# Performance work log

Measured on AMD Instinct MI355X. Metric: run time of the kernel, lower is better.

## Reference

```python
import jax, jax.numpy as jnp
import numpy as np

TAU = 0.5
EPS = 1e-8


def setup_inputs() -> dict:
    key = jax.random.key(0)
    k1, k2 = jax.random.split(key)
    N, D = 200000, 512
    z_pos = jax.random.normal(k1, (N, D), dtype=jnp.float32)
    W = jax.random.normal(k2, (D, D), dtype=jnp.float32) * (1.0 / np.sqrt(D))
    b = jnp.zeros((D,), dtype=jnp.float32)
    return {"z_pos": z_pos, "W": W, "b": b}


def reference(z_pos, W, b):
    # sample_centroid: softmax-weighted centroid (computed on detached embeddings)
    h = jax.lax.stop_gradient(z_pos)
    init_c = h.mean(axis=0)                              # [D]
    d2 = jnp.sum((h - init_c[None, :]) ** 2, axis=1)     # [N]
    w = jax.nn.softmax(-d2 / TAU)                        # [N]
    c = jnp.sum(h * w[:, None], axis=0)                  # [D]

    # SimNet: dist = 1 - cosine_similarity(proj(x), c)
    x_proj = z_pos @ W.T + b                             # [N, D]
    x_norm = jnp.maximum(jnp.linalg.norm(x_proj, axis=-1), EPS)  # [N]
    c_norm = jnp.maximum(jnp.linalg.norm(c), EPS)
    cos = (x_proj @ c) / (x_norm * c_norm)               # [N]
    dist = 1.0 - cos
    return dist
```

## Files before the change

### kernel.cpp

```cpp
#include <hip/hip_runtime.h>
#include <hip/hip_bf16.h>
#include <math.h>

#define DD 512
#define EPSF 1e-8f
#define BM 128
#define BN 128
#define BK 32
#define FBIG 3.402823466e+38f
#define NPART 2048

typedef __bf16 bf16_t;
typedef __bf16 bf16x4_t __attribute__((ext_vector_type(4)));
typedef __bf16 bf16x8_t __attribute__((ext_vector_type(8)));
typedef float f32x4 __attribute__((ext_vector_type(4)));

__device__ inline float bf2f(unsigned short u) {
    return __uint_as_float(((unsigned int)u) << 16);
}

__global__ void k_convW(const float* __restrict__ W, bf16_t* __restrict__ Wb) {
    int i = blockIdx.x * blockDim.x + threadIdx.x;
    float4 v = ((const float4*)W)[i];
    bf16x4_t o;
    o[0] = (bf16_t)v.x; o[1] = (bf16_t)v.y; o[2] = (bf16_t)v.z; o[3] = (bf16_t)v.w;
    ((bf16x4_t*)Wb)[i] = o;
}

template<bool CONV>
__global__ void k_colsum(const float* __restrict__ z, bf16_t* __restrict__ zb,
                         float* __restrict__ part, int N, int rpb) {
    int t = threadIdx.x;
    int b = blockIdx.x;
    int col4 = t & 127, sub = t >> 7;
    int r0 = b * rpb, r1 = min(r0 + rpb, N);
    const float4* z4 = (const float4*)z;
    float4 acc = make_float4(0.f, 0.f, 0.f, 0.f);
    #pragma unroll 4
    for (int r = r0 + sub; r < r1; r += 2) {
        float4 v = z4[(size_t)r * 128 + col4];
        if (CONV) {
            bf16x4_t o;
            o[0] = (bf16_t)v.x; o[1] = (bf16_t)v.y; o[2] = (bf16_t)v.z; o[3] = (bf16_t)v.w;
            ((bf16x4_t*)zb)[(size_t)r * 128 + col4] = o;
        }
        acc.x += v.x; acc.y += v.y; acc.z += v.z; acc.w += v.w;
    }
    __shared__ float4 sm[128];
    if (sub == 1) sm[col4] = acc;
    __syncthreads();
    if (sub == 0) {
        float4 o = sm[col4];
        acc.x += o.x; acc.y += o.y; acc.z += o.z; acc.w += o.w;
        ((float4*)(part + (size_t)b * DD))[col4] = acc;
    }
}

__global__ void k_wcolsum_f(const float* __restrict__ z, const float* __restrict__ d2,
                            const float* __restrict__ d2min, const float* __restrict__ sinvp,
                            float* __restrict__ part, int N, int rpb) {
    int t = threadIdx.x;
    int b = blockIdx.x;
    int col4 = t & 127, sub = t >> 7;
    int r0 = b * rpb, r1 = min(r0 + rpb, N);
    float m  = d2min[0];
    float is = sinvp[0];
    const float4* z4 = (const float4*)z;
    float4 acc = make_float4(0.f, 0.f, 0.f, 0.f);
    #pragma unroll 4
    for (int r = r0 + sub; r < r1; r += 2) {
        float w = __expf(-2.0f * (d2[r] - m)) * is;
        float4 v = z4[(size_t)r * 128 + col4];
        acc.x += w * v.x; acc.y += w * v.y; acc.z += w * v.z; acc.w += w * v.w;
    }
    __shared__ float4 sm[128];
    if (sub == 1) sm[col4] = acc;
    __syncthreads();
    if (sub == 0) {
        float4 o = sm[col4];
        acc.x += o.x; acc.y += o.y; acc.z += o.z; acc.w += o.w;
        ((float4*)(part + (size_t)b * DD))[col4] = acc;
    }
}

__global__ void k_wcolsum_b(const bf16_t* __restrict__ zb, const float* __restrict__ d2,
                            const float* __restrict__ d2min, const float* __restrict__ sinvp,
                            float* __restrict__ part, int N, int rpb) {
    int t = threadIdx.x;
    int b = blockIdx.x;
    int col4 = t & 127, sub = t >> 7;
    int r0 = b * rpb, r1 = min(r0 + rpb, N);
    float m  = d2min[0];
    float is = sinvp[0];
    const ushort4* z4 = (const ushort4*)zb;
    float4 acc = make_float4(0.f, 0.f, 0.f, 0.f);
    #pragma unroll 8
    for (int r = r0 + sub; r < r1; r += 2) {
        float w = __expf(-2.0f * (d2[r] - m)) * is;
        ushort4 u = z4[(size_t)r * 128 + col4];
        acc.x += w * bf2f(u.x); acc.y += w * bf2f(u.y);
        acc.z += w * bf2f(u.z); acc.w += w * bf2f(u.w);
    }
    __shared__ float4 sm[128];
    if (sub == 1) sm[col4] = acc;
    __syncthreads();
    if (sub == 0) {
        float4 o = sm[col4];
        acc.x += o.x; acc.y += o.y; acc.z += o.z; acc.w += o.w;
        ((float4*)(part + (size_t)b * DD))[col4] = acc;
    }
}

__global__ void k_reduceP(const float* __restrict__ part, float* __restrict__ outv, float scale) {
    __shared__ float sm[256];
    int j = blockIdx.x;
    int t = threadIdx.x;
    float s = 0.f;
    #pragma unroll
    for (int p = 0; p < NPART / 256; ++p) s += part[(size_t)(p * 256 + t) * DD + j];
    sm[t] = s;
    __syncthreads();
    for (int st = 128; st > 0; st >>= 1) {
        if (t < st) sm[t] += sm[t + st];
        __syncthreads();
    }
    if (t == 0) outv[j] = sm[0] * scale;
}

__global__ void k_d2s(const float* __restrict__ z, const float* __restrict__ cbar,
                      float* __restrict__ d2, float* __restrict__ mpart,
                      float* __restrict__ spart, int N) {
    int t = threadIdx.x;
    int lane = t & 63, wv = t >> 6;
    int l15 = lane & 15, r4 = lane >> 4;
    const float4* c4 = (const float4*)cbar;
    float4 cf[8];
    #pragma unroll
    for (int q = 0; q < 8; ++q) cf[q] = c4[q * 16 + l15];
    int gw = (blockIdx.x * 256 + t) >> 6;
    int nw = (gridDim.x * 256) >> 6;
    float m = FBIG, s = 0.f;
    #pragma unroll 2
    for (int r = gw * 4 + r4; r < N; r += nw * 4) {
        const float4* zr = (const float4*)(z + (size_t)r * DD);
        float sum = 0.f;
        #pragma unroll
        for (int q = 0; q < 8; ++q) {
            float4 v = zr[q * 16 + l15];
            float d;
            d = v.x - cf[q].x; sum += d * d;
            d = v.y - cf[q].y; sum += d * d;
            d = v.z - cf[q].z; sum += d * d;
            d = v.w - cf[q].w; sum += d * d;
        }
        #pragma unroll
        for (int off = 1; off < 16; off <<= 1) sum += __shfl_xor(sum, off, 64);
        if (l15 == 0) d2[r] = sum;
        float nm = fminf(m, sum);
        s = s * __expf(-2.0f * (m - nm)) + __expf(-2.0f * (sum - nm));
        m = nm;
    }
    #pragma unroll
    for (int off = 16; off < 64; off <<= 1) {
        float m2 = __shfl_xor(m, off, 64);
        float s2 = __shfl_xor(s, off, 64);
        float nm = fminf(m, m2);
        s = s * __expf(-2.0f * (m - nm)) + s2 * __expf(-2.0f * (m2 - nm));
        m = nm;
    }
    __shared__ float smm[4], sms[4];
    if (lane == 0) { smm[wv] = m; sms[wv] = s; }
    __syncthreads();
    if (t == 0) {
        float M = fminf(fminf(smm[0], smm[1]), fminf(smm[2], smm[3]));
        float S = 0.f;
        #pragma unroll
        for (int i = 0; i < 4; ++i) S += sms[i] * __expf(-2.0f * (smm[i] - M));
        mpart[blockIdx.x] = M;
        spart[blockIdx.x] = S;
    }
}

__global__ void k_combine(const float* __restrict__ mpart, const float* __restrict__ spart,
                          float* __restrict__ d2min, float* __restrict__ sinvp) {
    __shared__ float smm[256], sms[256];
    int t = threadIdx.x;
    float M = FBIG, S = 0.f;
    for (int i = t; i < NPART; i += 256) {
        float m2 = mpart[i], s2 = spart[i];
        float nm = fminf(M, m2);
        S = S * __expf(-2.0f * (M - nm)) + s2 * __expf(-2.0f * (m2 - nm));
        M = nm;
    }
    smm[t] = M; sms[t] = S;
    __syncthreads();
    for (int st = 128; st > 0; st >>= 1) {
        if (t < st) {
            float m2 = smm[t + st], s2 = sms[t + st];
            float nm = fminf(smm[t], m2);
            sms[t] = sms[t] * __expf(-2.0f * (smm[t] - nm)) + s2 * __expf(-2.0f * (m2 - nm));
            smm[t] = nm;
        }
        __syncthreads();
    }
    if (t == 0) { d2min[0] = smm[0]; sinvp[0] = 1.0f / sms[0]; }
}

__global__ void k_cnorm(const float* __restrict__ cvec, float* __restrict__ outp) {
    __shared__ float sm[512];
    float v = cvec[threadIdx.x];
    sm[threadIdx.x] = v * v;
    __syncthreads();
    for (int st = 256; st > 0; st >>= 1) {
        if (threadIdx.x < st) sm[threadIdx.x] += sm[threadIdx.x + st];
        __syncthreads();
    }
    if (threadIdx.x == 0) outp[0] = 1.0f / fmaxf(sqrtf(sm[0]), EPSF);
}

template<bool ZB>
__global__ __launch_bounds__(256, 4) void k_gemm(
    const float* __restrict__ z, const bf16_t* __restrict__ zb,
    const bf16_t* __restrict__ Wb, const float* __restrict__ bvec,
    const float* __restrict__ cvec, float* __restrict__ sqp, float* __restrict__ dtp,
    int N, int npad)
{
    __shared__ bf16_t As[BM * BK];
    __shared__ bf16_t Bs[BN * BK];
    __shared__ float psq[BM][2];
    __shared__ float pdt[BM][2];

    const int t    = threadIdx.x;
    const int lane = t & 63;
    const int wv   = t >> 6;
    const int wr   = wv >> 1;
    const int wc   = wv & 1;
    const int quad = lane >> 4;
    const int l15  = lane & 15;
    const int cb   = blockIdx.x;
    const int row0 = blockIdx.y * BM;

    const bf16_t* bp = Wb + (size_t)(cb * BN + (t >> 2)) * DD + (t & 3) * 8;
    const bf16_t* ap = zb + (size_t)(row0 + (t >> 2)) * DD + (t & 3) * 8;

    const int arow = t >> 1;
    const int ah   = t & 1;
    int rowe = row0 + arow; if (rowe >= N) rowe = N - 1;
    const float4* zp4 = (const float4*)(z + (size_t)rowe * DD + ah * 16);

    f32x4 acc[4][4];
    #pragma unroll
    for (int a = 0; a < 4; ++a)
        #pragma unroll
        for (int b = 0; b < 4; ++b) acc[a][b] = (f32x4){0.f, 0.f, 0.f, 0.f};

    float4 v0, v1, v2, v3;
    if (!ZB) { v0 = zp4[0]; v1 = zp4[1]; v2 = zp4[2]; v3 = zp4[3]; }

    for (int kc = 0; kc < DD; kc += BK) {
        if (kc) __syncthreads();

        #pragma unroll
        for (int q = 0; q < 2; ++q) {
            int ldsoff = __builtin_amdgcn_readfirstlane(q * 4096 + wv * 1024);
            __builtin_amdgcn_global_load_lds(
                (const __attribute__((address_space(1))) unsigned int*)(const void*)(bp + (size_t)q * 64 * DD + kc),
                (__attribute__((address_space(3))) unsigned int*)(void*)((char*)Bs + ldsoff),
                16, 0, 0);
        }
        if (ZB) {
            #pragma unroll
            for (int q = 0; q < 2; ++q) {
                int ldsoff = __builtin_amdgcn_readfirstlane(q * 4096 + wv * 1024);
                __builtin_amdgcn_global_load_lds(
                    (const __attribute__((address_space(1))) unsigned int*)(const void*)(ap + (size_t)q * 64 * DD + kc),
                    (__attribute__((address_space(3))) unsigned int*)(void*)((char*)As + ldsoff),
                    16, 0, 0);
            }
        } else {
            bf16x8_t lo, hi;
            lo[0]=(bf16_t)v0.x; lo[1]=(bf16_t)v0.y; lo[2]=(bf16_t)v0.z; lo[3]=(bf16_t)v0.w;
            lo[4]=(bf16_t)v1.x; lo[5]=(bf16_t)v1.y; lo[6]=(bf16_t)v1.z; lo[7]=(bf16_t)v1.w;
            hi[0]=(bf16_t)v2.x; hi[1]=(bf16_t)v2.y; hi[2]=(bf16_t)v2.z; hi[3]=(bf16_t)v2.w;
            hi[4]=(bf16_t)v3.x; hi[5]=(bf16_t)v3.y; hi[6]=(bf16_t)v3.z; hi[7]=(bf16_t)v3.w;
            *(bf16x8_t*)(As + arow * BK + ah * 16)     = lo;
            *(bf16x8_t*)(As + arow * BK + ah * 16 + 8) = hi;
        }

        __syncthreads();

        if (!ZB && kc + BK < DD) {
            int kf = (kc + BK) >> 2;
            v0 = zp4[kf]; v1 = zp4[kf + 1]; v2 = zp4[kf + 2]; v3 = zp4[kf + 3];
        }

        bf16x8_t af[4];
        #pragma unroll
        for (int rt = 0; rt < 4; ++rt)
            af[rt] = *(const bf16x8_t*)(As + (wr * 64 + rt * 16 + l15) * BK + quad * 8);
        #pragma unroll
        for (int ct = 0; ct < 4; ++ct) {
            bf16x8_t bfv = *(const bf16x8_t*)(Bs + (wc * 64 + ct * 16 + l15) * BK + quad * 8);
            #pragma unroll
            for (int rt = 0; rt < 4; ++rt)
                acc[rt][ct] = __builtin_amdgcn_mfma_f32_16x16x32_bf16(af[rt], bfv, acc[rt][ct], 0, 0, 0);
        }
    }

    float bc[4], cc[4];
    #pragma unroll
    for (int ct = 0; ct < 4; ++ct) {
        int col = cb * BN + wc * 64 + ct * 16 + l15;
        bc[ct] = bvec[col];
        cc[ct] = cvec[col];
    }
    #pragma unroll
    for (int rt = 0; rt < 4; ++rt) {
        #pragma unroll
        for (int rg = 0; rg < 4; ++rg) {
            float sq = 0.f, dt = 0.f;
            #pragma unroll
            for (int ct = 0; ct < 4; ++ct) {
                float x = acc[rt][ct][rg] + bc[ct];
                sq += x * x;
                dt += x * cc[ct];
            }
            #pragma unroll
            for (int off = 1; off < 16; off <<= 1) {
                sq += __shfl_xor(sq, off, 64);
                dt += __shfl_xor(dt, off, 64);
            }
            if (l15 == 0) {
                int rl = wr * 64 + rt * 16 + quad * 4 + rg;
                psq[rl][wc] = sq;
                pdt[rl][wc] = dt;
            }
        }
    }
    __syncthreads();
    if (t < BM) {
        int r = row0 + t;
        if (r < N) {
            sqp[(size_t)cb * npad + r] = psq[t][0] + psq[t][1];
            dtp[(size_t)cb * npad + r] = pdt[t][0] + pdt[t][1];
        }
    }
}

__global__ void k_final(const float* __restrict__ sqp, const float* __restrict__ dtp,
                        const float* __restrict__ cninv, float* __restrict__ out,
                        int N, int npad) {
    int r = blockIdx.x * blockDim.x + threadIdx.x;
    if (r < N) {
        float sq = sqp[r] + sqp[(size_t)npad + r] + sqp[2 * (size_t)npad + r] + sqp[3 * (size_t)npad + r];
        float dt = dtp[r] + dtp[(size_t)npad + r] + dtp[2 * (size_t)npad + r] + dtp[3 * (size_t)npad + r];
        out[r] = 1.0f - dt * cninv[0] / fmaxf(sqrtf(sq), EPSF);
    }
}

extern "C" void kernel_launch(void* const* d_in, const int* in_sizes, int n_in,
                              void* d_out, int out_size, void* d_ws, size_t ws_size,
                              hipStream_t stream)
{
    const float* z = (const float*)d_in[0];
    const float* W = (const float*)d_in[1];
    const float* b = (const float*)d_in[2];
    float* out = (float*)d_out;
    int N = in_sizes[0] / DD;
    int npad = ((N + BM - 1) / BM) * BM;

    float* ws = (float*)d_ws;
    size_t off = 0;
    float* part  = ws + off; off += (size_t)NPART * DD;
    float* cbar  = ws + off; off += DD;
    float* d2    = ws + off; off += (size_t)npad;
    float* mpart = ws + off; off += NPART;
    float* spart = ws + off; off += NPART;
    float* d2min = ws + off; off += 1;
    float* sinvp = ws + off; off += 1;
    float* cvec  = ws + off; off += DD;
    float* cninv = ws + off; off += 1;
    off = (off + 3) & ~(size_t)3;
    float* sqp   = ws + off; off += (size_t)4 * npad;
    float* dtp   = ws + off; off += (size_t)4 * npad;
    bf16_t* Wb   = (bf16_t*)(ws + off); off += (size_t)DD * DD / 2;
    bf16_t* zb   = (bf16_t*)(ws + off);
    size_t need_bytes = (off + (size_t)npad * DD / 2) * sizeof(float);
    const bool use_zb = ws_size >= need_bytes;

    int rpb = (N + NPART - 1) / NPART;

    k_convW<<<256, 256, 0, stream>>>(W, Wb);
    if (use_zb) k_colsum<true ><<<NPART, 256, 0, stream>>>(z, zb, part, N, rpb);
    else        k_colsum<false><<<NPART, 256, 0, stream>>>(z, zb, part, N, rpb);
    k_reduceP<<<DD, 256, 0, stream>>>(part, cbar, 1.0f / (float)N);
    k_d2s<<<NPART, 256, 0, stream>>>(z, cbar, d2, mpart, spart, N);
    k_combine<<<1, 256, 0, stream>>>(mpart, spart, d2min, sinvp);
    if (use_zb) k_wcolsum_b<<<NPART, 256, 0, stream>>>(zb, d2, d2min, sinvp, part, N, rpb);
    else        k_wcolsum_f<<<NPART, 256, 0, stream>>>(z,  d2, d2min, sinvp, part, N, rpb);
    k_reduceP<<<DD, 256, 0, stream>>>(part, cvec, 1.0f);
    k_cnorm<<<1, DD, 0, stream>>>(cvec, cninv);
    dim3 grid(4, npad / BM);
    if (use_zb) k_gemm<true ><<<grid, 256, 0, stream>>>(z, zb, Wb, b, cvec, sqp, dtp, N, npad);
    else        k_gemm<false><<<grid, 256, 0, stream>>>(z, zb, Wb, b, cvec, sqp, dtp, N, npad);
    k_final<<<(N + 255) / 256, 256, 0, stream>>>(sqp, dtp, cninv, out, N, npad);
}
```

Baseline: 904.0 us.

## Fuse distance, online softmax and weighted centroid into one pass over z

Merges the d2/softmax-stats kernel and the separate weighted column-sum kernel into a single pass. It keeps an online-softmax running max and rescales per-thread weighted accumulators, so z (or its bf16 copy) is read once instead of twice. The per-block partial centroids are then rescaled by per-block weights in a new weighted reduction kernel. The GEMM epilogue also shortens its shuffle reduction and stores more partials in shared memory. This costs more registers in the fused kernel (eight float4 accumulators plus loaded values) and rescaling work whenever the running max changes.

```diff
diff --git a/kernel.cpp b/kernel.cpp
--- a/kernel.cpp
+++ b/kernel.cpp
@@ -14,10 +14,6 @@
 typedef __bf16 bf16x4_t __attribute__((ext_vector_type(4)));
 typedef __bf16 bf16x8_t __attribute__((ext_vector_type(8)));
 typedef float f32x4 __attribute__((ext_vector_type(4)));
-
-__device__ inline float bf2f(unsigned short u) {
-    return __uint_as_float(((unsigned int)u) << 16);
-}
 
 __global__ void k_convW(const float* __restrict__ W, bf16_t* __restrict__ Wb) {
     int i = blockIdx.x * blockDim.x + threadIdx.x;
@@ -56,61 +52,6 @@
     }
 }
 
-__global__ void k_wcolsum_f(const float* __restrict__ z, const float* __restrict__ d2,
-                            const float* __restrict__ d2min, const float* __restrict__ sinvp,
-                            float* __restrict__ part, int N, int rpb) {
-    int t = threadIdx.x;
-    int b = blockIdx.x;
-    int col4 = t & 127, sub = t >> 7;
-    int r0 = b * rpb, r1 = min(r0 + rpb, N);
-    float m  = d2min[0];
-    float is = sinvp[0];
-    const float4* z4 = (const float4*)z;
-    float4 acc = make_float4(0.f, 0.f, 0.f, 0.f);
-    #pragma unroll 4
-    for (int r = r0 + sub; r < r1; r += 2) {
-        float w = __expf(-2.0f * (d2[r] - m)) * is;
-        float4 v = z4[(size_t)r * 128 + col4];
-        acc.x += w * v.x; acc.y += w * v.y; acc.z += w * v.z; acc.w += w * v.w;
-    }
-    __shared__ float4 sm[128];
-    if (sub == 1) sm[col4] = acc;
-    __syncthreads();
-    if (sub == 0) {
-        float4 o = sm[col4];
-        acc.x += o.x; acc.y += o.y; acc.z += o.z; acc.w += o.w;
-        ((float4*)(part + (size_t)b * DD))[col4] = acc;
-    }
-}
-
-__global__ void k_wcolsum_b(const bf16_t* __restrict__ zb, const float* __restrict__ d2,
-                            const float* __restrict__ d2min, const float* __restrict__ sinvp,
-                            float* __restrict__ part, int N, int rpb) {
-    int t = threadIdx.x;
-    int b = blockIdx.x;
-    int col4 = t & 127, sub = t >> 7;
-    int r0 = b * rpb, r1 = min(r0 + rpb, N);
-    float m  = d2min[0];
-    float is = sinvp[0];
-    const ushort4* z4 = (const ushort4*)zb;
-    float4 acc = make_float4(0.f, 0.f, 0.f, 0.f);
-    #pragma unroll 8
-    for (int r = r0 + sub; r < r1; r += 2) {
-        float w = __expf(-2.0f * (d2[r] - m)) * is;
-        ushort4 u = z4[(size_t)r * 128 + col4];
-        acc.x += w * bf2f(u.x); acc.y += w * bf2f(u.y);
-        acc.z += w * bf2f(u.z); acc.w += w * bf2f(u.w);
-    }
-    __shared__ float4 sm[128];
-    if (sub == 1) sm[col4] = acc;
-    __syncthreads();
-    if (sub == 0) {
-        float4 o = sm[col4];
-        acc.x += o.x; acc.y += o.y; acc.z += o.z; acc.w += o.w;
-        ((float4*)(part + (size_t)b * DD))[col4] = acc;
-    }
-}
-
 __global__ void k_reduceP(const float* __restrict__ part, float* __restrict__ outv, float scale) {
     __shared__ float sm[256];
     int j = blockIdx.x;
@@ -127,83 +68,152 @@
     if (t == 0) outv[j] = sm[0] * scale;
 }
 
-__global__ void k_d2s(const float* __restrict__ z, const float* __restrict__ cbar,
-                      float* __restrict__ d2, float* __restrict__ mpart,
-                      float* __restrict__ spart, int N) {
+__global__ __launch_bounds__(256, 4) void k_d2w(
+    const float* __restrict__ z, const float* __restrict__ cbar,
+    float* __restrict__ part, float* __restrict__ mpart,
+    float* __restrict__ spart, int N)
+{
+    __shared__ float4 cs[128];
+    __shared__ float4 vsm[4][128];
+    __shared__ float wm[4], wsv[4];
     int t = threadIdx.x;
     int lane = t & 63, wv = t >> 6;
     int l15 = lane & 15, r4 = lane >> 4;
-    const float4* c4 = (const float4*)cbar;
-    float4 cf[8];
-    #pragma unroll
-    for (int q = 0; q < 8; ++q) cf[q] = c4[q * 16 + l15];
+    if (t < 128) cs[t] = ((const float4*)cbar)[t];
+    __syncthreads();
+
     int gw = (blockIdx.x * 256 + t) >> 6;
     int nw = (gridDim.x * 256) >> 6;
     float m = FBIG, s = 0.f;
-    #pragma unroll 2
+    float4 acc[8];
+    #pragma unroll
+    for (int q = 0; q < 8; ++q) acc[q] = make_float4(0.f, 0.f, 0.f, 0.f);
+
     for (int r = gw * 4 + r4; r < N; r += nw * 4) {
         const float4* zr = (const float4*)(z + (size_t)r * DD);
+        float4 vv[8];
         float sum = 0.f;
         #pragma unroll
         for (int q = 0; q < 8; ++q) {
             float4 v = zr[q * 16 + l15];
+            float4 c = cs[q * 16 + l15];
+            vv[q] = v;
             float d;
-            d = v.x - cf[q].x; sum += d * d;
-            d = v.y - cf[q].y; sum += d * d;
-            d = v.z - cf[q].z; sum += d * d;
-            d = v.w - cf[q].w; sum += d * d;
+            d = v.x - c.x; sum += d * d;
+            d = v.y - c.y; sum += d * d;
+            d = v.z - c.z; sum += d * d;
+            d = v.w - c.w; sum += d * d;
         }
         #pragma unroll
         for (int off = 1; off < 16; off <<= 1) sum += __shfl_xor(sum, off, 64);
-        if (l15 == 0) d2[r] = sum;
-        float nm = fminf(m, sum);
-        s = s * __expf(-2.0f * (m - nm)) + __expf(-2.0f * (sum - nm));
-        m = nm;
+        float w;
+        if (sum < m) {
+            float f = __expf(-2.0f * (m - sum));
+            s *= f;
+            #pragma unroll
+            for (int q = 0; q < 8; ++q) {
+                acc[q].x *= f; acc[q].y *= f; acc[q].z *= f; acc[q].w *= f;
+            }
+            m = sum;
+            w = 1.0f;
+        } else {
+            w = __expf(-2.0f * (sum - m));
+        }
+        s += w;
+        #pragma unroll
+        for (int q = 0; q < 8; ++q) {
+            acc[q].x += w * vv[q].x; acc[q].y += w * vv[q].y;
+            acc[q].z += w * vv[q].z; acc[q].w += w * vv[q].w;
+        }
+    }
+
+    float mw = fminf(m, __shfl_xor(m, 16, 64));
+    mw = fminf(mw, __shfl_xor(mw, 32, 64));
+    float f = __expf(-2.0f * (m - mw));
+    s *= f;
+    #pragma unroll
+    for (int q = 0; q < 8; ++q) {
+        acc[q].x *= f; acc[q].y *= f; acc[q].z *= f; acc[q].w *= f;
     }
     #pragma unroll
     for (int off = 16; off < 64; off <<= 1) {
-        float m2 = __shfl_xor(m, off, 64);
-        float s2 = __shfl_xor(s, off, 64);
-        float nm = fminf(m, m2);
-        s = s * __expf(-2.0f * (m - nm)) + s2 * __expf(-2.0f * (m2 - nm));
-        m = nm;
-    }
-    __shared__ float smm[4], sms[4];
-    if (lane == 0) { smm[wv] = m; sms[wv] = s; }
-    __syncthreads();
-    if (t == 0) {
-        float M = fminf(fminf(smm[0], smm[1]), fminf(smm[2], smm[3]));
-        float S = 0.f;
-        #pragma unroll
-        for (int i = 0; i < 4; ++i) S += sms[i] * __expf(-2.0f * (smm[i] - M));
-        mpart[blockIdx.x] = M;
-        spart[blockIdx.x] = S;
-    }
-}
-
-__global__ void k_combine(const float* __restrict__ mpart, const float* __restrict__ spart,
-                          float* __restrict__ d2min, float* __restrict__ sinvp) {
+        s += __shfl_xor(s, off, 64);
+        #pragma unroll
+        for (int q = 0; q < 8; ++q) {
+            acc[q].x += __shfl_xor(acc[q].x, off, 64);
+            acc[q].y += __shfl_xor(acc[q].y, off, 64);
+            acc[q].z += __shfl_xor(acc[q].z, off, 64);
+            acc[q].w += __shfl_xor(acc[q].w, off, 64);
+        }
+    }
+    if (lane < 16) {
+        #pragma unroll
+        for (int q = 0; q < 8; ++q) vsm[wv][q * 16 + l15] = acc[q];
+        if (lane == 0) { wm[wv] = mw; wsv[wv] = s; }
+    }
+    __syncthreads();
+    if (t < 128) {
+        float M = fminf(fminf(wm[0], wm[1]), fminf(wm[2], wm[3]));
+        float4 o = make_float4(0.f, 0.f, 0.f, 0.f);
+        #pragma unroll
+        for (int w2 = 0; w2 < 4; ++w2) {
+            float fw = __expf(-2.0f * (wm[w2] - M));
+            float4 a = vsm[w2][t];
+            o.x += fw * a.x; o.y += fw * a.y; o.z += fw * a.z; o.w += fw * a.w;
+        }
+        ((float4*)(part + (size_t)blockIdx.x * DD))[t] = o;
+        if (t == 0) {
+            float S = 0.f;
+            #pragma unroll
+            for (int w2 = 0; w2 < 4; ++w2) S += wsv[w2] * __expf(-2.0f * (wm[w2] - M));
+            mpart[blockIdx.x] = M;
+            spart[blockIdx.x] = S;
+        }
+    }
+}
+
+__global__ void k_combine2(const float* __restrict__ mpart, const float* __restrict__ spart,
+                           float* __restrict__ wscale) {
     __shared__ float smm[256], sms[256];
     int t = threadIdx.x;
-    float M = FBIG, S = 0.f;
-    for (int i = t; i < NPART; i += 256) {
-        float m2 = mpart[i], s2 = spart[i];
-        float nm = fminf(M, m2);
-        S = S * __expf(-2.0f * (M - nm)) + s2 * __expf(-2.0f * (m2 - nm));
-        M = nm;
-    }
-    smm[t] = M; sms[t] = S;
+    float M = FBIG;
+    for (int i = t; i < NPART; i += 256) M = fminf(M, mpart[i]);
+    smm[t] = M;
     __syncthreads();
     for (int st = 128; st > 0; st >>= 1) {
-        if (t < st) {
-            float m2 = smm[t + st], s2 = sms[t + st];
-            float nm = fminf(smm[t], m2);
-            sms[t] = sms[t] * __expf(-2.0f * (smm[t] - nm)) + s2 * __expf(-2.0f * (m2 - nm));
-            smm[t] = nm;
-        }
-        __syncthreads();
-    }
-    if (t == 0) { d2min[0] = smm[0]; sinvp[0] = 1.0f / sms[0]; }
+        if (t < st) smm[t] = fminf(smm[t], smm[t + st]);
+        __syncthreads();
+    }
+    M = smm[0];
+    float S = 0.f;
+    for (int i = t; i < NPART; i += 256) S += spart[i] * __expf(-2.0f * (mpart[i] - M));
+    sms[t] = S;
+    __syncthreads();
+    for (int st = 128; st > 0; st >>= 1) {
+        if (t < st) sms[t] += sms[t + st];
+        __syncthreads();
+    }
+    float inv = 1.0f / sms[0];
+    for (int i = t; i < NPART; i += 256) wscale[i] = __expf(-2.0f * (mpart[i] - M)) * inv;
+}
+
+__global__ void k_reducePW(const float* __restrict__ part, const float* __restrict__ wscale,
+                           float* __restrict__ outv) {
+    __shared__ float sm[256];
+    int j = blockIdx.x, t = threadIdx.x;
+    float s = 0.f;
+    #pragma unroll
+    for (int p = 0; p < NPART / 256; ++p) {
+        int b = p * 256 + t;
+        s += part[(size_t)b * DD + j] * wscale[b];
+    }
+    sm[t] = s;
+    __syncthreads();
+    for (int st = 128; st > 0; st >>= 1) {
+        if (t < st) sm[t] += sm[t + st];
+        __syncthreads();
+    }
+    if (t == 0) outv[j] = sm[0];
 }
 
 __global__ void k_cnorm(const float* __restrict__ cvec, float* __restrict__ outp) {
@@ -227,8 +237,8 @@
 {
     __shared__ bf16_t As[BM * BK];
     __shared__ bf16_t Bs[BN * BK];
-    __shared__ float psq[BM][2];
-    __shared__ float pdt[BM][2];
+    __shared__ float psq[BM][8];
+    __shared__ float pdt[BM][8];
 
     const int t    = threadIdx.x;
     const int lane = t & 63;
@@ -325,15 +335,12 @@
                 sq += x * x;
                 dt += x * cc[ct];
             }
-            #pragma unroll
-            for (int off = 1; off < 16; off <<= 1) {
-                sq += __shfl_xor(sq, off, 64);
-                dt += __shfl_xor(dt, off, 64);
-            }
-            if (l15 == 0) {
+            sq += __shfl_xor(sq, 1, 64); dt += __shfl_xor(dt, 1, 64);
+            sq += __shfl_xor(sq, 2, 64); dt += __shfl_xor(dt, 2, 64);
+            if ((l15 & 3) == 0) {
                 int rl = wr * 64 + rt * 16 + quad * 4 + rg;
-                psq[rl][wc] = sq;
-                pdt[rl][wc] = dt;
+                psq[rl][wc * 4 + (l15 >> 2)] = sq;
+                pdt[rl][wc * 4 + (l15 >> 2)] = dt;
             }
         }
     }
@@ -341,8 +348,11 @@
     if (t < BM) {
         int r = row0 + t;
         if (r < N) {
-            sqp[(size_t)cb * npad + r] = psq[t][0] + psq[t][1];
-            dtp[(size_t)cb * npad + r] = pdt[t][0] + pdt[t][1];
+            float sq = 0.f, dt = 0.f;
+            #pragma unroll
+            for (int i = 0; i < 8; ++i) { sq += psq[t][i]; dt += pdt[t][i]; }
+            sqp[(size_t)cb * npad + r] = sq;
+            dtp[(size_t)cb * npad + r] = dt;
         }
     }
 }
@@ -371,20 +381,18 @@
 
     float* ws = (float*)d_ws;
     size_t off = 0;
-    float* part  = ws + off; off += (size_t)NPART * DD;
-    float* cbar  = ws + off; off += DD;
-    float* d2    = ws + off; off += (size_t)npad;
-    float* mpart = ws + off; off += NPART;
-    float* spart = ws + off; off += NPART;
-    float* d2min = ws + off; off += 1;
-    float* sinvp = ws + off; off += 1;
-    float* cvec  = ws + off; off += DD;
-    float* cninv = ws + off; off += 1;
+    float* part   = ws + off; off += (size_t)NPART * DD;
+    float* cbar   = ws + off; off += DD;
+    float* mpart  = ws + off; off += NPART;
+    float* spart  = ws + off; off += NPART;
+    float* wscale = ws + off; off += NPART;
+    float* cvec   = ws + off; off += DD;
+    float* cninv  = ws + off; off += 1;
     off = (off + 3) & ~(size_t)3;
-    float* sqp   = ws + off; off += (size_t)4 * npad;
-    float* dtp   = ws + off; off += (size_t)4 * npad;
-    bf16_t* Wb   = (bf16_t*)(ws + off); off += (size_t)DD * DD / 2;
-    bf16_t* zb   = (bf16_t*)(ws + off);
+    float* sqp    = ws + off; off += (size_t)4 * npad;
+    float* dtp    = ws + off; off += (size_t)4 * npad;
+    bf16_t* Wb    = (bf16_t*)(ws + off); off += (size_t)DD * DD / 2;
+    bf16_t* zb    = (bf16_t*)(ws + off);
     size_t need_bytes = (off + (size_t)npad * DD / 2) * sizeof(float);
     const bool use_zb = ws_size >= need_bytes;
 
@@ -394,11 +402,9 @@
     if (use_zb) k_colsum<true ><<<NPART, 256, 0, stream>>>(z, zb, part, N, rpb);
     else        k_colsum<false><<<NPART, 256, 0, stream>>>(z, zb, part, N, rpb);
     k_reduceP<<<DD, 256, 0, stream>>>(part, cbar, 1.0f / (float)N);
-    k_d2s<<<NPART, 256, 0, stream>>>(z, cbar, d2, mpart, spart, N);
-    k_combine<<<1, 256, 0, stream>>>(mpart, spart, d2min, sinvp);
-    if (use_zb) k_wcolsum_b<<<NPART, 256, 0, stream>>>(zb, d2, d2min, sinvp, part, N, rpb);
-    else        k_wcolsum_f<<<NPART, 256, 0, stream>>>(z,  d2, d2min, sinvp, part, N, rpb);
-    k_reduceP<<<DD, 256, 0, stream>>>(part, cvec, 1.0f);
+    k_d2w<<<NPART, 256, 0, stream>>>(z, cbar, part, mpart, spart, N);
+    k_combine2<<<1, 256, 0, stream>>>(mpart, spart, wscale);
+    k_reducePW<<<DD, 256, 0, stream>>>(part, wscale, cvec);
     k_cnorm<<<1, DD, 0, stream>>>(cvec, cninv);
     dim3 grid(4, npad / BM);
     if (use_zb) k_gemm<true ><<<grid, 256, 0, stream>>>(z, zb, Wb, b, cvec, sqp, dtp, N, npad);
```

Result: faster. 878.8 us (-2.8%).
